# Performance work log

Measured on AMD Instinct MI355X. Metric: run time of the kernel, lower is better.

The kernel has to match this reference:

```python
import jax, jax.numpy as jnp
import numpy as np

N = 4608      # total nodes (48 graphs x 96 nodes)
B = 48
NPG = 96
D = 512       # vec_dim
XD = 16       # x_dim
E = N * 32    # GAT edges
L = 6         # GAT layers


def _w(k, shape, fan_in):
    return jax.random.normal(k, shape, jnp.float32) * (1.0 / np.sqrt(fan_in))


def setup_inputs() -> dict:
    key = jax.random.key(0)
    ks = jax.random.split(key, 24)
    x = jax.random.normal(ks[0], (N, XD), jnp.float32)
    xyz = jax.random.normal(ks[1], (N, 3), jnp.float32)
    edge_index = jax.random.randint(ks[2], (2, E), 0, N, dtype=jnp.int32)
    ptr = (jnp.arange(B + 1) * NPG).astype(jnp.int32)
    # complete graph with replacement per segment (torch.combinations order: i<=j)
    i, j = np.triu_indices(NPG)
    offs = (np.arange(B) * NPG)[:, None]
    cloud_edge_index = jnp.asarray(
        np.stack([(i[None, :] + offs).reshape(-1), (j[None, :] + offs).reshape(-1)]),
        jnp.int32)
    return {
        'x': x, 'edge_index': edge_index, 'ptr': ptr, 'xyz': xyz,
        'cloud_edge_index': cloud_edge_index,
        'x_proj_w': _w(ks[3], (XD, D), XD), 'x_proj_b': jnp.zeros((D,), jnp.float32),
        'gat_wl': _w(ks[4], (L, D, D), D), 'gat_bl': jnp.zeros((L, D), jnp.float32),
        'gat_wr': _w(ks[5], (L, D, D), D), 'gat_br': jnp.zeros((L, D), jnp.float32),
        'gat_att': _w(ks[6], (L, D), D), 'gat_bias': jnp.zeros((L, D), jnp.float32),
        'gat_ln_g': jnp.ones((L - 1, D), jnp.float32), 'gat_ln_b': jnp.zeros((L - 1, D), jnp.float32),
        'cg_xyz_w': _w(ks[7], (3, D), 3),
        'cg_bn_g': jnp.ones((D,), jnp.float32), 'cg_bn_b': jnp.zeros((D,), jnp.float32),
        'cg_lin1_w': _w(ks[8], (D, D), D), 'cg_lin1_b': jnp.zeros((D,), jnp.float32),
        'cg_ln_g': jnp.ones((D,), jnp.float32), 'cg_ln_b': jnp.zeros((D,), jnp.float32),
        'lin_w': _w(ks[9], (D, D), D), 'lin_b': jnp.zeros((D,), jnp.float32),
        'bn_g': jnp.ones((D,), jnp.float32), 'bn_b': jnp.zeros((D,), jnp.float32),
    }


def _batchnorm(t, g, b):
    mu = t.mean(0)
    v = ((t - mu) ** 2).mean(0)
    return (t - mu) / jnp.sqrt(v + 1e-5) * g + b


def _forward(x, edge_index, cloud_edge_index, x_proj_w, x_proj_b, gat_wl, gat_bl,
             gat_wr, gat_br, gat_att, gat_bias, gat_ln_g, gat_ln_b, cg_xyz_w,
             cg_bn_g, cg_bn_b, cg_lin1_w, cg_lin1_b, cg_ln_g, cg_ln_b,
             lin_w, lin_b, bn_g, bn_b, xyz):
    n = x.shape[0]
    h = x @ x_proj_w + x_proj_b  # [N, D]
    # ---- GATv2 stack (heads=1, self-loops added, eval mode: no dropout) ----
    loops = jnp.arange(n, dtype=edge_index.dtype)
    ei = jnp.concatenate([edge_index, jnp.stack([loops, loops])], axis=1)
    src, dst = ei[0], ei[1]
    xg = h
    for l in range(L):
        xl = xg @ gat_wl[l] + gat_bl[l]
        xr = xg @ gat_wr[l] + gat_br[l]
        e = jax.nn.leaky_relu(xl[src] + xr[dst], 0.2) @ gat_att[l]  # [E+N]
        m = jax.ops.segment_max(e, dst, num_segments=n)
        ew = jnp.exp(e - m[dst])
        den = jax.ops.segment_sum(ew, dst, num_segments=n)
        alpha = ew / den[dst]
        out = jax.ops.segment_sum(alpha[:, None] * xl[src], dst, num_segments=n) + gat_bias[l]
        if l < L - 1:
            # PyG LayerNorm, mode='graph', batch=None: normalize over all elements
            mu = out.mean()
            sd = jnp.sqrt(((out - mu) ** 2).mean())
            out = (out - mu) / (sd + 1e-5) * gat_ln_g[l] + gat_ln_b[l]
            out = jax.nn.relu(out)
        xg = out
    # ---- CloudGraph (complete graph gather-compute-scatter) ----
    a, b = cloud_edge_index[0], cloud_edge_index[1]
    rx = h[a] - h[b]          # [Ec, D]
    rz = xyz[a] - xyz[b]      # [Ec, 3]
    sq = (rz ** 2).sum(-1)
    dist = jnp.where(sq > 0, jnp.sqrt(jnp.where(sq > 0, sq, 1.0)), 0.0)
    w = jnp.exp(-dist)[:, None]
    p1 = jax.ops.segment_sum(jax.nn.relu((w * rx) @ cg_lin1_w + cg_lin1_b), a, num_segments=n)
    mu1 = p1.mean(-1, keepdims=True)
    v1 = ((p1 - mu1) ** 2).mean(-1, keepdims=True)
    ln1 = (p1 - mu1) / jnp.sqrt(v1 + 1e-5) * cg_ln_g + cg_ln_b
    p2 = jax.ops.segment_sum(jax.nn.relu(rz @ cg_xyz_w), a, num_segments=n)
    xc = h + ln1 + _batchnorm(p2, cg_bn_g, cg_bn_b)
    # ---- fuse + final norm ----
    return _batchnorm((h + xg + xc) @ lin_w + lin_b, bn_g, bn_b)


def reference(x, edge_index, ptr, xyz, cloud_edge_index, x_proj_w, x_proj_b,
              gat_wl, gat_bl, gat_wr, gat_br, gat_att, gat_bias, gat_ln_g,
              gat_ln_b, cg_xyz_w, cg_bn_g, cg_bn_b, cg_lin1_w, cg_lin1_b,
              cg_ln_g, cg_ln_b, lin_w, lin_b, bn_g, bn_b):
    return _forward(x, edge_index, cloud_edge_index, x_proj_w, x_proj_b, gat_wl,
                    gat_bl, gat_wr, gat_br, gat_att, gat_bias, gat_ln_g,
                    gat_ln_b, cg_xyz_w, cg_bn_g, cg_bn_b, cg_lin1_w, cg_lin1_b,
                    cg_ln_g, cg_ln_b, lin_w, lin_b, bn_g, bn_b, xyz)
```

## Files before the change

kernel.cpp:

```cpp
#include <hip/hip_runtime.h>
#include <hip/hip_bf16.h>

#define NN 4608
#define BG 48
#define NPG 96
#define DD 512
#define XDIM 16
#define EREAL 147456
#define NLAYER 6
#define NK 262144
#define TRIU 4656

typedef __hip_bfloat16 bf16;
typedef short short8 __attribute__((ext_vector_type(8)));
typedef short short4v __attribute__((ext_vector_type(4)));
typedef float f32x4 __attribute__((ext_vector_type(4)));

__device__ __forceinline__ float s2f(short s) {
  return __uint_as_float(((unsigned int)(unsigned short)s) << 16);
}
__device__ __forceinline__ short f2bs(float f) {
  bf16 h = __float2bfloat16(f);
  short s;
  __builtin_memcpy(&s, &h, 2);
  return s;
}

__global__ __launch_bounds__(256) void k_wt(const float* __restrict__ wl,
                                            const float* __restrict__ wr,
                                            const float* __restrict__ cg,
                                            const float* __restrict__ lin,
                                            bf16* __restrict__ Wt,
                                            int* __restrict__ counts,
                                            float* __restrict__ statsAll) {
  if (blockIdx.z == 0) {
    int id = (blockIdx.y * 16 + blockIdx.x) * 256 + threadIdx.x;
    if (id < NN) counts[id] = 0;
    if (id < 5 * 32) statsAll[id] = 0.f;
  }
  __shared__ float tile[32][33];
  int z = blockIdx.z;
  const float* src = (z < 6) ? wl + (size_t)z * NK
                   : (z < 12) ? wr + (size_t)(z - 6) * NK
                   : (z == 12) ? cg : lin;
  bf16* dst = Wt + (size_t)z * NK;
  int c = threadIdx.x & 31;
  int r0 = threadIdx.x >> 5;
  int bx = blockIdx.x * 32, by = blockIdx.y * 32;
#pragma unroll
  for (int i = 0; i < 4; i++) {
    int r = r0 + i * 8;
    tile[r][c] = src[(size_t)(by + r) * 512 + bx + c];
  }
  __syncthreads();
#pragma unroll
  for (int i = 0; i < 4; i++) {
    int r = r0 + i * 8;
    dst[(size_t)(bx + r) * 512 + by + c] = __float2bfloat16(tile[c][r]);
  }
}

__global__ void k_xproj(const float* __restrict__ x, const float* __restrict__ w,
                        const float* __restrict__ b, const int* __restrict__ ei,
                        const float* __restrict__ xyz,
                        bf16* __restrict__ h_bf, int* __restrict__ counts,
                        float* __restrict__ ep) {
  int i = blockIdx.x * blockDim.x + threadIdx.x;
  if (i >= NN * DD) return;
  if (i < EREAL) atomicAdd(&counts[ei[EREAL + i]], 1);
  if (i < NN * NPG) {
    int n = i / NPG, e = i - n * NPG;
    int p = n % NPG;
    if (e < NPG - p) {
      int g = n / NPG;
      int slot = g * TRIU + p * NPG - (p * (p - 1)) / 2 + e;
      int j = n + e;
      float dx = xyz[n * 3] - xyz[j * 3];
      float dy = xyz[n * 3 + 1] - xyz[j * 3 + 1];
      float dz = xyz[n * 3 + 2] - xyz[j * 3 + 2];
      float sq = dx * dx + dy * dy + dz * dz;
      float dist = (sq > 0.f) ? sqrtf(sq) : 0.f;
      float4 v;
      v.x = dx; v.y = dy; v.z = dz; v.w = __expf(-dist);
      *(float4*)&ep[(size_t)slot * 4] = v;
    }
  }
  int n = i >> 9, d = i & 511;
  float acc = b[d];
#pragma unroll
  for (int k = 0; k < XDIM; k++) acc += x[n * XDIM + k] * w[k * DD + d];
  h_bf[i] = __float2bfloat16(acc);
}

__global__ void k_scan(const int* __restrict__ counts, int* offsets, int* cursor) {
  __shared__ int part[256];
  __shared__ int pre[256];
  int t = threadIdx.x;
  int base = t * 18;
  int s = 0;
#pragma unroll
  for (int i = 0; i < 18; i++) s += counts[base + i];
  part[t] = s;
  __syncthreads();
  if (t == 0) {
    int r = 0;
    for (int i = 0; i < 256; i++) { pre[i] = r; r += part[i]; }
  }
  __syncthreads();
  int run = pre[t];
#pragma unroll
  for (int i = 0; i < 18; i++) {
    offsets[base + i] = run;
    cursor[base + i] = run;
    run += counts[base + i];
  }
  if (t == 0) offsets[NN] = EREAL;
}
__global__ void k_scatter(const int* __restrict__ ei, int* cursor, int* ssrc) {
  int e = blockIdx.x * blockDim.x + threadIdx.x;
  if (e < EREAL) {
    int s = ei[e], d = ei[EREAL + e];
    int pos = atomicAdd(&cursor[d], 1);
    ssrc[pos] = s;
  }
}

__global__ __launch_bounds__(256) void k_gemm(
    const bf16* __restrict__ Abf,
    const bf16* __restrict__ B0, const bf16* __restrict__ B1,
    const float* __restrict__ bias0, const float* __restrict__ bias1,
    float* __restrict__ C0, float* __restrict__ C1,
    bf16* __restrict__ Cb0, bf16* __restrict__ Cb1,
    const float* __restrict__ statsIn,
    const float* __restrict__ lng, const float* __restrict__ lnb,
    float* __restrict__ zptr, int zn,
    float* __restrict__ csum, float* __restrict__ csq) {
  if (zptr && blockIdx.x == 0 && blockIdx.y == 0 && blockIdx.z == 0) {
    for (int i = threadIdx.x; i < zn; i += 256) zptr[i] = 0.f;
  }
  __shared__ __align__(16) bf16 As[128 * 40];
  __shared__ __align__(16) bf16 Bs[64 * 40];
  __shared__ float cs[64], cq[64];
  const bf16* B = blockIdx.z ? B1 : B0;
  const float* bias = blockIdx.z ? bias1 : bias0;
  float* C = blockIdx.z ? C1 : C0;
  bf16* Cb = blockIdx.z ? Cb1 : Cb0;
  int tid = threadIdx.x;
  int m0 = blockIdx.x * 128, n0 = blockIdx.y * 64;
  int lane = tid & 63, wid = tid >> 6;
  int mh = (wid >> 1) * 64, nh = (wid & 1) * 32;
  int l15 = lane & 15, quad = lane >> 4;

  if (csum && tid < 64) { cs[tid] = 0.f; cq[tid] = 0.f; }

  float mu = 0.f, inv = 1.f;
  if (statsIn) {
    float s = 0.f, ss = 0.f;
#pragma unroll
    for (int i = 0; i < 16; i++) { s += statsIn[i]; ss += statsIn[16 + i]; }
    const float invM = 1.f / ((float)NN * (float)DD);
    mu = s * invM;
    float var = ss * invM - mu * mu;
    float sd = sqrtf(fmaxf(var, 0.f));
    inv = 1.f / (sd + 1e-5f);
  }

  f32x4 acc[4][2];
#pragma unroll
  for (int mt = 0; mt < 4; mt++)
#pragma unroll
    for (int nt = 0; nt < 2; nt++) acc[mt][nt] = (f32x4)0.f;

  for (int k0 = 0; k0 < 512; k0 += 32) {
    if (statsIn) {
#pragma unroll
      for (int it = 0; it < 2; it++) {
        int idx = tid + it * 256;
        int row = idx >> 2, kc = (idx & 3) * 8;
        short8 raw = *(const short8*)&Abf[(size_t)(m0 + row) * 512 + k0 + kc];
        float4 ga = *(const float4*)&lng[k0 + kc];
        float4 gb = *(const float4*)&lng[k0 + kc + 4];
        float4 ba = *(const float4*)&lnb[k0 + kc];
        float4 bb = *(const float4*)&lnb[k0 + kc + 4];
        float gg[8] = {ga.x, ga.y, ga.z, ga.w, gb.x, gb.y, gb.z, gb.w};
        float bv[8] = {ba.x, ba.y, ba.z, ba.w, bb.x, bb.y, bb.z, bb.w};
        short8 pk;
#pragma unroll
        for (int k = 0; k < 8; k++) {
          float t = fmaxf((s2f(raw[k]) - mu) * inv * gg[k] + bv[k], 0.f);
          pk[k] = f2bs(t);
        }
        *(short8*)&As[row * 40 + kc] = pk;
      }
    } else {
#pragma unroll
      for (int it = 0; it < 2; it++) {
        int idx = tid + it * 256;
        int row = idx >> 2, kc = (idx & 3) * 8;
        *(short8*)&As[row * 40 + kc] =
            *(const short8*)&Abf[(size_t)(m0 + row) * 512 + k0 + kc];
      }
    }
    {
      int row = tid >> 2, kc = (tid & 3) * 8;
      *(short8*)&Bs[row * 40 + kc] =
          *(const short8*)&B[(size_t)(n0 + row) * 512 + k0 + kc];
    }
    __syncthreads();
    short8 af[4], bfr[2];
#pragma unroll
    for (int mt = 0; mt < 4; mt++)
      af[mt] = *(const short8*)&As[(mh + mt * 16 + l15) * 40 + quad * 8];
#pragma unroll
    for (int nt = 0; nt < 2; nt++)
      bfr[nt] = *(const short8*)&Bs[(nh + nt * 16 + l15) * 40 + quad * 8];
#pragma unroll
    for (int mt = 0; mt < 4; mt++)
#pragma unroll
      for (int nt = 0; nt < 2; nt++)
        acc[mt][nt] = __builtin_amdgcn_mfma_f32_16x16x32_bf16(
            af[mt], bfr[nt], acc[mt][nt], 0, 0, 0);
    __syncthreads();
  }
  float colS[2] = {0.f, 0.f}, colQ[2] = {0.f, 0.f};
#pragma unroll
  for (int mt = 0; mt < 4; mt++) {
#pragma unroll
    for (int nt = 0; nt < 2; nt++) {
      int col = n0 + nh + nt * 16 + l15;
      float bv = bias ? bias[col] : 0.f;
#pragma unroll
      for (int r = 0; r < 4; r++) {
        int row = m0 + mh + mt * 16 + quad * 4 + r;
        float v = acc[mt][nt][r] + bv;
        if (C) C[(size_t)row * 512 + col] = v;
        if (Cb) Cb[(size_t)row * 512 + col] = __float2bfloat16(v);
        if (csum) { colS[nt] += v; colQ[nt] += v * v; }
      }
    }
  }
  if (csum) {
#pragma unroll
    for (int nt = 0; nt < 2; nt++) {
      atomicAdd(&cs[nh + nt * 16 + l15], colS[nt]);
      atomicAdd(&cq[nh + nt * 16 + l15], colQ[nt]);
    }
    __syncthreads();
    if (tid < 64) {
      atomicAdd(&csum[n0 + tid], cs[tid]);
      atomicAdd(&csq[n0 + tid], cq[tid]);
    }
  }
}

__global__ __launch_bounds__(256) void k_gat_edge(const bf16* __restrict__ xl,
                                                  const bf16* __restrict__ xr,
                                                  const float* __restrict__ att,
                                                  const float* __restrict__ bias,
                                                  const int* __restrict__ offs,
                                                  const int* __restrict__ ssrc,
                                                  bf16* __restrict__ out,
                                                  float* __restrict__ statsOut) {
  __shared__ float redS[4], redSS[4];
  int wave = (blockIdx.x * blockDim.x + threadIdx.x) >> 6;
  int lane = threadIdx.x & 63;
  int wid = threadIdx.x >> 6;
  if (wave < NN) {
    int n = wave;
    int base = lane * 8;
    float xrv[8], attv[8], acc[8];
    short8 xr8 = *(const short8*)&xr[(size_t)n * 512 + base];
#pragma unroll
    for (int k = 0; k < 8; k++) {
      xrv[k] = s2f(xr8[k]);
      attv[k] = att[base + k];
    }
    float m0, lsum;
    {
      short8 a8 = *(const short8*)&xl[(size_t)n * 512 + base];
      float sc0 = 0.f;
#pragma unroll
      for (int k = 0; k < 8; k++) {
        float v = s2f(a8[k]);
        acc[k] = v;
        float t = v + xrv[k];
        t = (t > 0.f) ? t : 0.2f * t;
        sc0 += attv[k] * t;
      }
#pragma unroll
      for (int off = 32; off >= 1; off >>= 1) sc0 += __shfl_xor(sc0, off, 64);
      m0 = sc0;
      lsum = 1.f;
    }
    int e0 = offs[n], e1 = offs[n + 1];
    int e = e0;
    for (; e + 3 < e1; e += 4) {
      int s0 = ssrc[e], s1 = ssrc[e + 1], s2 = ssrc[e + 2], s3 = ssrc[e + 3];
      short8 a0 = *(const short8*)&xl[(size_t)s0 * 512 + base];
      short8 a1 = *(const short8*)&xl[(size_t)s1 * 512 + base];
      short8 a2 = *(const short8*)&xl[(size_t)s2 * 512 + base];
      short8 a3 = *(const short8*)&xl[(size_t)s3 * 512 + base];
      float x0[8], x1[8], x2[8], x3[8];
      float c0 = 0.f, c1 = 0.f, c2 = 0.f, c3 = 0.f;
#pragma unroll
      for (int k = 0; k < 8; k++) {
        float v0 = s2f(a0[k]), v1 = s2f(a1[k]), v2 = s2f(a2[k]), v3 = s2f(a3[k]);
        x0[k] = v0; x1[k] = v1; x2[k] = v2; x3[k] = v3;
        float t0 = v0 + xrv[k]; t0 = (t0 > 0.f) ? t0 : 0.2f * t0; c0 += attv[k] * t0;
        float t1 = v1 + xrv[k]; t1 = (t1 > 0.f) ? t1 : 0.2f * t1; c1 += attv[k] * t1;
        float t2 = v2 + xrv[k]; t2 = (t2 > 0.f) ? t2 : 0.2f * t2; c2 += attv[k] * t2;
        float t3 = v3 + xrv[k]; t3 = (t3 > 0.f) ? t3 : 0.2f * t3; c3 += attv[k] * t3;
      }
#pragma unroll
      for (int off = 32; off >= 1; off >>= 1) {
        c0 += __shfl_xor(c0, off, 64);
        c1 += __shfl_xor(c1, off, 64);
        c2 += __shfl_xor(c2, off, 64);
        c3 += __shfl_xor(c3, off, 64);
      }
      float p0 = __expf(c0 - m0), p1 = __expf(c1 - m0);
      float p2 = __expf(c2 - m0), p3 = __expf(c3 - m0);
      lsum += p0 + p1 + p2 + p3;
#pragma unroll
      for (int k = 0; k < 8; k++)
        acc[k] += p0 * x0[k] + p1 * x1[k] + p2 * x2[k] + p3 * x3[k];
    }
    for (; e < e1; ++e) {
      int s0 = ssrc[e];
      short8 a8 = *(const short8*)&xl[(size_t)s0 * 512 + base];
      float x0[8];
      float sc0 = 0.f;
#pragma unroll
      for (int k = 0; k < 8; k++) {
        float v0 = s2f(a8[k]);
        x0[k] = v0;
        float t0 = v0 + xrv[k];
        t0 = (t0 > 0.f) ? t0 : 0.2f * t0;
        sc0 += attv[k] * t0;
      }
#pragma unroll
      for (int off = 32; off >= 1; off >>= 1) sc0 += __shfl_xor(sc0, off, 64);
      float p0 = __expf(sc0 - m0);
      lsum += p0;
#pragma unroll
      for (int k = 0; k < 8; k++) acc[k] += p0 * x0[k];
    }
    float inv = 1.f / lsum;
    float o[8];
    float s = 0.f, ss = 0.f;
    short8 o8;
#pragma unroll
    for (int k = 0; k < 8; k++) {
      o[k] = acc[k] * inv + bias[base + k];
      s += o[k];
      ss += o[k] * o[k];
      o8[k] = f2bs(o[k]);
    }
    *(short8*)&out[(size_t)n * 512 + base] = o8;
    if (statsOut) {
#pragma unroll
      for (int off = 32; off >= 1; off >>= 1) {
        s += __shfl_xor(s, off, 64);
        ss += __shfl_xor(ss, off, 64);
      }
      if (lane == 0) { redS[wid] = s; redSS[wid] = ss; }
    }
  }
  if (statsOut) {
    __syncthreads();
    if (threadIdx.x == 0) {
      float a = redS[0] + redS[1] + redS[2] + redS[3];
      float b = redSS[0] + redSS[1] + redSS[2] + redSS[3];
      int slot = blockIdx.x & 15;
      atomicAdd(&statsOut[slot], a);
      atomicAdd(&statsOut[16 + slot], b);
    }
  }
}

__global__ __launch_bounds__(256) void k_cloud(const bf16* __restrict__ g1,
                                               const float* __restrict__ ep,
                                               const float* __restrict__ lin1b,
                                               const float* __restrict__ w3,
                                               float* __restrict__ p1,
                                               float* __restrict__ p2) {
  int w = (blockIdx.x * blockDim.x + threadIdx.x) >> 6;
  int lane = threadIdx.x & 63;
  if (w >= NN) return;
  int hf = w & 1;
  int pi = w >> 1;
  int g = pi / 48, pp = pi % 48;
  int d0 = hf * 256 + lane * 4;
  float4 bb = *(const float4*)&lin1b[d0];
  float4 w30 = *(const float4*)&w3[d0];
  float4 w31 = *(const float4*)&w3[512 + d0];
  float4 w32 = *(const float4*)&w3[1024 + d0];
  float bbv[4] = {bb.x, bb.y, bb.z, bb.w};
  float w0v[4] = {w30.x, w30.y, w30.z, w30.w};
  float w1v[4] = {w31.x, w31.y, w31.z, w31.w};
  float w2v[4] = {w32.x, w32.y, w32.z, w32.w};

#pragma unroll
  for (int half = 0; half < 2; half++) {
    int p = half ? (NPG - 1 - pp) : pp;
    int n = g * NPG + p;
    int cnt = NPG - p;
    int slot0 = g * TRIU + p * NPG - (p * (p - 1)) / 2;
    float gi[4], a1[4], a2[4];
    short4v gi4 = *(const short4v*)&g1[(size_t)n * 512 + d0];
#pragma unroll
    for (int k = 0; k < 4; k++) {
      gi[k] = s2f(gi4[k]);
      a1[k] = 0.f;
      a2[k] = 0.f;
    }
    int e = 0;
    for (; e + 1 < cnt; e += 2) {
      float4 pa = *(const float4*)&ep[(size_t)(slot0 + e) * 4];
      float4 pb = *(const float4*)&ep[(size_t)(slot0 + e + 1) * 4];
      short4v ga = *(const short4v*)&g1[(size_t)(n + e) * 512 + d0];
      short4v gb = *(const short4v*)&g1[(size_t)(n + e + 1) * 512 + d0];
#pragma unroll
      for (int k = 0; k < 4; k++) {
        float t = fmaf(pa.w, gi[k] - s2f(ga[k]), bbv[k]);
        a1[k] += fmaxf(t, 0.f);
        float u = fmaf(pb.w, gi[k] - s2f(gb[k]), bbv[k]);
        a1[k] += fmaxf(u, 0.f);
        float t2 = pa.x * w0v[k] + pa.y * w1v[k] + pa.z * w2v[k];
        a2[k] += fmaxf(t2, 0.f);
        float u2 = pb.x * w0v[k] + pb.y * w1v[k] + pb.z * w2v[k];
        a2[k] += fmaxf(u2, 0.f);
      }
    }
    if (e < cnt) {
      float4 pa = *(const float4*)&ep[(size_t)(slot0 + e) * 4];
      short4v ga = *(const short4v*)&g1[(size_t)(n + e) * 512 + d0];
#pragma unroll
      for (int k = 0; k < 4; k++) {
        float t = fmaf(pa.w, gi[k] - s2f(ga[k]), bbv[k]);
        a1[k] += fmaxf(t, 0.f);
        float t2 = pa.x * w0v[k] + pa.y * w1v[k] + pa.z * w2v[k];
        a2[k] += fmaxf(t2, 0.f);
      }
    }
    float4 o1, o2;
    o1.x = a1[0]; o1.y = a1[1]; o1.z = a1[2]; o1.w = a1[3];
    o2.x = a2[0]; o2.y = a2[1]; o2.z = a2[2]; o2.w = a2[3];
    *(float4*)&p1[(size_t)n * 512 + d0] = o1;
    *(float4*)&p2[(size_t)n * 512 + d0] = o2;
  }
}

__global__ __launch_bounds__(256) void k_cloud_epi(
    const float* __restrict__ p1, const float* __restrict__ p2,
    const bf16* __restrict__ h_bf, const bf16* __restrict__ xg_bf,
    const float* __restrict__ colsum, const float* __restrict__ colsq,
    const float* __restrict__ lng, const float* __restrict__ lnb,
    const float* __restrict__ bng, const float* __restrict__ bnb,
    bf16* __restrict__ s_bf, float* __restrict__ zptr) {
  if (blockIdx.x == 0) {
    for (int i = threadIdx.x; i < 1024; i += 256) zptr[i] = 0.f;
  }
  int wave = (blockIdx.x * blockDim.x + threadIdx.x) >> 6;
  int lane = threadIdx.x & 63;
  if (wave >= NN) return;
  int n = wave;
  size_t rb = (size_t)n * 512 + lane * 8;
  int base = lane * 8;
  float v[8];
  float s = 0.f;
#pragma unroll
  for (int k = 0; k < 8; k++) {
    v[k] = p1[rb + k];
    s += v[k];
  }
#pragma unroll
  for (int off = 32; off >= 1; off >>= 1) s += __shfl_xor(s, off, 64);
  float mu = s * (1.f / 512.f);
  float ss = 0.f;
#pragma unroll
  for (int k = 0; k < 8; k++) {
    float t = v[k] - mu;
    ss += t * t;
  }
#pragma unroll
  for (int off = 32; off >= 1; off >>= 1) ss += __shfl_xor(ss, off, 64);
  float inv = 1.f / sqrtf(ss * (1.f / 512.f) + 1e-5f);
  short8 hb = *(const short8*)&h_bf[rb];
  short8 xb = *(const short8*)&xg_bf[rb];
  short8 o8;
#pragma unroll
  for (int k = 0; k < 8; k++) {
    int d = base + k;
    float ln1 = (v[k] - mu) * inv * lng[d] + lnb[d];
    float cmu = colsum[d] * (1.f / NN);
    float cvar = colsq[d] * (1.f / NN) - cmu * cmu;
    float cinv = 1.f / sqrtf(fmaxf(cvar, 0.f) + 1e-5f);
    float bnv = (p2[rb + k] - cmu) * cinv * bng[d] + bnb[d];
    float out = 2.f * s2f(hb[k]) + s2f(xb[k]) + ln1 + bnv;
    o8[k] = f2bs(out);
  }
  *(short8*)&s_bf[rb] = o8;
}

__global__ void k_col_reduce(const float* __restrict__ x, float* colsum, float* colsq) {
  int r0 = blockIdx.x * 128;
  int c0 = threadIdx.x;
  float s0 = 0.f, q0 = 0.f, s1 = 0.f, q1 = 0.f;
  for (int r = r0; r < r0 + 128; ++r) {
    float v = x[(size_t)r * 512 + c0];
    s0 += v;
    q0 += v * v;
    float w = x[(size_t)r * 512 + c0 + 256];
    s1 += w;
    q1 += w * w;
  }
  atomicAdd(&colsum[c0], s0);
  atomicAdd(&colsq[c0], q0);
  atomicAdd(&colsum[c0 + 256], s1);
  atomicAdd(&colsq[c0 + 256], q1);
}
__global__ void k_bn_out(const float* __restrict__ y, const float* __restrict__ colsum,
                         const float* __restrict__ colsq, const float* __restrict__ g,
                         const float* __restrict__ b, float* __restrict__ out) {
  int i = blockIdx.x * blockDim.x + threadIdx.x;
  if (i >= NN * DD) return;
  int d = i & 511;
  float mu = colsum[d] * (1.f / NN);
  float var = colsq[d] * (1.f / NN) - mu * mu;
  float inv = 1.f / sqrtf(fmaxf(var, 0.f) + 1e-5f);
  out[i] = (y[i] - mu) * inv * g[d] + b[d];
}

extern "C" void kernel_launch(void* const* d_in, const int* in_sizes, int n_in,
                              void* d_out, int out_size, void* d_ws, size_t ws_size,
                              hipStream_t stream) {
  const float* x = (const float*)d_in[0];
  const int* ei = (const int*)d_in[1];
  const float* xyz = (const float*)d_in[3];
  const float* x_proj_w = (const float*)d_in[5];
  const float* x_proj_b = (const float*)d_in[6];
  const float* gat_wl = (const float*)d_in[7];
  const float* gat_bl = (const float*)d_in[8];
  const float* gat_wr = (const float*)d_in[9];
  const float* gat_br = (const float*)d_in[10];
  const float* gat_att = (const float*)d_in[11];
  const float* gat_bias = (const float*)d_in[12];
  const float* gat_ln_g = (const float*)d_in[13];
  const float* gat_ln_b = (const float*)d_in[14];
  const float* cg_xyz_w = (const float*)d_in[15];
  const float* cg_bn_g = (const float*)d_in[16];
  const float* cg_bn_b = (const float*)d_in[17];
  const float* cg_lin1_w = (const float*)d_in[18];
  const float* cg_lin1_b = (const float*)d_in[19];
  const float* cg_ln_g = (const float*)d_in[20];
  const float* cg_ln_b = (const float*)d_in[21];
  const float* lin_w = (const float*)d_in[22];
  const float* lin_b = (const float*)d_in[23];
  const float* bn_g = (const float*)d_in[24];
  const float* bn_b = (const float*)d_in[25];

  const size_t ND = (size_t)NN * DD;
  char* w = (char*)d_ws;
  float* p1 = (float*)w;       w += ND * 4;
  float* p2 = (float*)w;       w += ND * 4;
  bf16* h_bf = (bf16*)w;       w += ND * 2;
  bf16* xg_bf = (bf16*)w;      w += ND * 2;
  bf16* xl_bf = (bf16*)w;      w += ND * 2;
  bf16* xr_bf = (bf16*)w;      w += ND * 2;
  bf16* Wt = (bf16*)w;         w += (size_t)14 * NK * 2;
  float* eparam = (float*)w;   w += (size_t)BG * TRIU * 16;
  int* counts = (int*)w;       w += NN * 4;
  int* offs = (int*)w;         w += (NN + 4) * 4;
  int* cursor = (int*)w;       w += NN * 4;
  int* ssrc = (int*)w;         w += EREAL * 4;
  float* statsAll = (float*)w; w += 5 * 32 * 4;
  float* colsum = (float*)w;   w += 512 * 4;
  float* colsq = (float*)w;    w += 512 * 4;
  float* colsum2 = (float*)w;  w += 512 * 4;
  float* colsq2 = (float*)w;   w += 512 * 4;
  float* y = p1;
  bf16* g1_bf = xl_bf;
  bf16* s_bf = h_bf;

  const int TPB = 256;
  const int ND_BLK = (int)((ND + TPB - 1) / TPB);

  k_wt<<<dim3(16, 16, 14), TPB, 0, stream>>>(gat_wl, gat_wr, cg_lin1_w, lin_w, Wt,
                                             counts, statsAll);
  k_xproj<<<ND_BLK, TPB, 0, stream>>>(x, x_proj_w, x_proj_b, ei, xyz, h_bf,
                                      counts, eparam);
  k_scan<<<1, 256, 0, stream>>>(counts, offs, cursor);
  k_scatter<<<(EREAL + TPB - 1) / TPB, TPB, 0, stream>>>(ei, cursor, ssrc);

  for (int l = 0; l < NLAYER; l++) {
    const bf16* A = (l == 0) ? h_bf : xg_bf;
    const float* sIn = (l > 0) ? statsAll + 32 * (l - 1) : nullptr;
    const float* lg = (l > 0) ? gat_ln_g + (l - 1) * DD : nullptr;
    const float* lb = (l > 0) ? gat_ln_b + (l - 1) * DD : nullptr;
    k_gemm<<<dim3(36, 8, 2), TPB, 0, stream>>>(
        A, Wt + (size_t)l * NK, Wt + (size_t)(6 + l) * NK,
        gat_bl + l * DD, gat_br + l * DD, nullptr, nullptr, xl_bf, xr_bf,
        sIn, lg, lb, nullptr, 0, nullptr, nullptr);
    float* sOut = (l < NLAYER - 1) ? statsAll + 32 * l : nullptr;
    k_gat_edge<<<NN / 4, TPB, 0, stream>>>(xl_bf, xr_bf, gat_att + l * DD,
                                           gat_bias + l * DD, offs, ssrc,
                                           xg_bf, sOut);
  }

  k_gemm<<<dim3(36, 8, 1), TPB, 0, stream>>>(
      h_bf, Wt + (size_t)12 * NK, Wt + (size_t)12 * NK, nullptr, nullptr,
      nullptr, nullptr, g1_bf, g1_bf, nullptr, nullptr, nullptr,
      colsum, 1024, nullptr, nullptr);
  k_cloud<<<NN / 4, TPB, 0, stream>>>(g1_bf, eparam, cg_lin1_b, cg_xyz_w, p1, p2);
  k_col_reduce<<<36, 256, 0, stream>>>(p2, colsum, colsq);
  k_cloud_epi<<<NN / 4, TPB, 0, stream>>>(p1, p2, h_bf, xg_bf, colsum, colsq,
                                          cg_ln_g, cg_ln_b, cg_bn_g, cg_bn_b,
                                          s_bf, colsum2);

  k_gemm<<<dim3(36, 8, 1), TPB, 0, stream>>>(
      s_bf, Wt + (size_t)13 * NK, Wt + (size_t)13 * NK, lin_b, lin_b,
      y, y, nullptr, nullptr, nullptr, nullptr, nullptr,
      nullptr, 0, colsum2, colsq2);
  k_bn_out<<<ND_BLK, TPB, 0, stream>>>(y, colsum2, colsq2, bn_g, bn_b,
                                       (float*)d_out);
}
```

Before: 598.7 us.

## Store GAT source features in fp8 and split cloud kernel across more waves

Result: no change. 597.8 us (-0.2%).

```diff
diff --git a/kernel.cpp b/kernel.cpp
--- a/kernel.cpp
+++ b/kernel.cpp
@@ -13,8 +13,8 @@
 
 typedef __hip_bfloat16 bf16;
 typedef short short8 __attribute__((ext_vector_type(8)));
-typedef short short4v __attribute__((ext_vector_type(4)));
 typedef float f32x4 __attribute__((ext_vector_type(4)));
+typedef float f32x2 __attribute__((ext_vector_type(2)));
 
 __device__ __forceinline__ float s2f(short s) {
   return __uint_as_float(((unsigned int)(unsigned short)s) << 16);
@@ -24,6 +24,14 @@
   short s;
   __builtin_memcpy(&s, &h, 2);
   return s;
+}
+__device__ __forceinline__ unsigned char f2f8(float v) {
+  return (unsigned char)(__builtin_amdgcn_cvt_pk_fp8_f32(v, v, 0, false) & 0xff);
+}
+__device__ __forceinline__ void f8x4(unsigned int w, float* o) {
+  f32x2 a = __builtin_amdgcn_cvt_pk_f32_fp8(w, false);
+  f32x2 b = __builtin_amdgcn_cvt_pk_f32_fp8(w, true);
+  o[0] = a[0]; o[1] = a[1]; o[2] = b[0]; o[3] = b[1];
 }
 
 __global__ __launch_bounds__(256) void k_wt(const float* __restrict__ wl,
@@ -131,6 +139,7 @@
     const float* __restrict__ bias0, const float* __restrict__ bias1,
     float* __restrict__ C0, float* __restrict__ C1,
     bf16* __restrict__ Cb0, bf16* __restrict__ Cb1,
+    unsigned char* __restrict__ Cf8_0, unsigned char* __restrict__ Cf8_1,
     const float* __restrict__ statsIn,
     const float* __restrict__ lng, const float* __restrict__ lnb,
     float* __restrict__ zptr, int zn,
@@ -145,6 +154,7 @@
   const float* bias = blockIdx.z ? bias1 : bias0;
   float* C = blockIdx.z ? C1 : C0;
   bf16* Cb = blockIdx.z ? Cb1 : Cb0;
+  unsigned char* Cf8 = blockIdx.z ? Cf8_1 : Cf8_0;
   int tid = threadIdx.x;
   int m0 = blockIdx.x * 128, n0 = blockIdx.y * 64;
   int lane = tid & 63, wid = tid >> 6;
@@ -235,6 +245,7 @@
         float v = acc[mt][nt][r] + bv;
         if (C) C[(size_t)row * 512 + col] = v;
         if (Cb) Cb[(size_t)row * 512 + col] = __float2bfloat16(v);
+        if (Cf8) Cf8[(size_t)row * 512 + col] = f2f8(v);
         if (csum) { colS[nt] += v; colQ[nt] += v * v; }
       }
     }
@@ -253,7 +264,7 @@
   }
 }
 
-__global__ __launch_bounds__(256) void k_gat_edge(const bf16* __restrict__ xl,
+__global__ __launch_bounds__(256) void k_gat_edge(const unsigned char* __restrict__ xl8,
                                                   const bf16* __restrict__ xr,
                                                   const float* __restrict__ att,
                                                   const float* __restrict__ bias,
@@ -277,13 +288,15 @@
     }
     float m0, lsum;
     {
-      short8 a8 = *(const short8*)&xl[(size_t)n * 512 + base];
+      uint2 q = *(const uint2*)&xl8[(size_t)n * 512 + base];
+      float xs[8];
+      f8x4(q.x, xs);
+      f8x4(q.y, xs + 4);
       float sc0 = 0.f;
 #pragma unroll
       for (int k = 0; k < 8; k++) {
-        float v = s2f(a8[k]);
-        acc[k] = v;
-        float t = v + xrv[k];
+        acc[k] = xs[k];
+        float t = xs[k] + xrv[k];
         t = (t > 0.f) ? t : 0.2f * t;
         sc0 += attv[k] * t;
       }
@@ -296,20 +309,22 @@
     int e = e0;
     for (; e + 3 < e1; e += 4) {
       int s0 = ssrc[e], s1 = ssrc[e + 1], s2 = ssrc[e + 2], s3 = ssrc[e + 3];
-      short8 a0 = *(const short8*)&xl[(size_t)s0 * 512 + base];
-      short8 a1 = *(const short8*)&xl[(size_t)s1 * 512 + base];
-      short8 a2 = *(const short8*)&xl[(size_t)s2 * 512 + base];
-      short8 a3 = *(const short8*)&xl[(size_t)s3 * 512 + base];
+      uint2 q0 = *(const uint2*)&xl8[(size_t)s0 * 512 + base];
+      uint2 q1 = *(const uint2*)&xl8[(size_t)s1 * 512 + base];
+      uint2 q2 = *(const uint2*)&xl8[(size_t)s2 * 512 + base];
+      uint2 q3 = *(const uint2*)&xl8[(size_t)s3 * 512 + base];
       float x0[8], x1[8], x2[8], x3[8];
+      f8x4(q0.x, x0); f8x4(q0.y, x0 + 4);
+      f8x4(q1.x, x1); f8x4(q1.y, x1 + 4);
+      f8x4(q2.x, x2); f8x4(q2.y, x2 + 4);
+      f8x4(q3.x, x3); f8x4(q3.y, x3 + 4);
       float c0 = 0.f, c1 = 0.f, c2 = 0.f, c3 = 0.f;
 #pragma unroll
       for (int k = 0; k < 8; k++) {
-        float v0 = s2f(a0[k]), v1 = s2f(a1[k]), v2 = s2f(a2[k]), v3 = s2f(a3[k]);
-        x0[k] = v0; x1[k] = v1; x2[k] = v2; x3[k] = v3;
-        float t0 = v0 + xrv[k]; t0 = (t0 > 0.f) ? t0 : 0.2f * t0; c0 += attv[k] * t0;
-        float t1 = v1 + xrv[k]; t1 = (t1 > 0.f) ? t1 : 0.2f * t1; c1 += attv[k] * t1;
-        float t2 = v2 + xrv[k]; t2 = (t2 > 0.f) ? t2 : 0.2f * t2; c2 += attv[k] * t2;
-        float t3 = v3 + xrv[k]; t3 = (t3 > 0.f) ? t3 : 0.2f * t3; c3 += attv[k] * t3;
+        float t0 = x0[k] + xrv[k]; t0 = (t0 > 0.f) ? t0 : 0.2f * t0; c0 += attv[k] * t0;
+        float t1 = x1[k] + xrv[k]; t1 = (t1 > 0.f) ? t1 : 0.2f * t1; c1 += attv[k] * t1;
+        float t2 = x2[k] + xrv[k]; t2 = (t2 > 0.f) ? t2 : 0.2f * t2; c2 += attv[k] * t2;
+        float t3 = x3[k] + xrv[k]; t3 = (t3 > 0.f) ? t3 : 0.2f * t3; c3 += attv[k] * t3;
       }
 #pragma unroll
       for (int off = 32; off >= 1; off >>= 1) {
@@ -327,14 +342,14 @@
     }
     for (; e < e1; ++e) {
       int s0 = ssrc[e];
-      short8 a8 = *(const short8*)&xl[(size_t)s0 * 512 + base];
+      uint2 q = *(const uint2*)&xl8[(size_t)s0 * 512 + base];
       float x0[8];
+      f8x4(q.x, x0);
+      f8x4(q.y, x0 + 4);
       float sc0 = 0.f;
 #pragma unroll
       for (int k = 0; k < 8; k++) {
-        float v0 = s2f(a8[k]);
-        x0[k] = v0;
-        float t0 = v0 + xrv[k];
+        float t0 = x0[k] + xrv[k];
         t0 = (t0 > 0.f) ? t0 : 0.2f * t0;
         sc0 += attv[k] * t0;
       }
@@ -386,19 +401,15 @@
                                                float* __restrict__ p2) {
   int w = (blockIdx.x * blockDim.x + threadIdx.x) >> 6;
   int lane = threadIdx.x & 63;
-  if (w >= NN) return;
-  int hf = w & 1;
-  int pi = w >> 1;
+  if (w >= NN * 2) return;
+  int qf = w & 3;
+  int pi = w >> 2;
   int g = pi / 48, pp = pi % 48;
-  int d0 = hf * 256 + lane * 4;
-  float4 bb = *(const float4*)&lin1b[d0];
-  float4 w30 = *(const float4*)&w3[d0];
-  float4 w31 = *(const float4*)&w3[512 + d0];
-  float4 w32 = *(const float4*)&w3[1024 + d0];
-  float bbv[4] = {bb.x, bb.y, bb.z, bb.w};
-  float w0v[4] = {w30.x, w30.y, w30.z, w30.w};
-  float w1v[4] = {w31.x, w31.y, w31.z, w31.w};
-  float w2v[4] = {w32.x, w32.y, w32.z, w32.w};
+  int d0 = qf * 128 + lane * 2;
+  float bb0 = lin1b[d0], bb1 = lin1b[d0 + 1];
+  float w00 = w3[d0], w01 = w3[d0 + 1];
+  float w10 = w3[512 + d0], w11 = w3[512 + d0 + 1];
+  float w20 = w3[1024 + d0], w21 = w3[1024 + d0 + 1];
 
 #pragma unroll
   for (int half = 0; half < 2; half++) {
@@ -406,48 +417,40 @@
     int n = g * NPG + p;
     int cnt = NPG - p;
     int slot0 = g * TRIU + p * NPG - (p * (p - 1)) / 2;
-    float gi[4], a1[4], a2[4];
-    short4v gi4 = *(const short4v*)&g1[(size_t)n * 512 + d0];
-#pragma unroll
-    for (int k = 0; k < 4; k++) {
-      gi[k] = s2f(gi4[k]);
-      a1[k] = 0.f;
-      a2[k] = 0.f;
-    }
+    unsigned int giw = *(const unsigned int*)&g1[(size_t)n * 512 + d0];
+    float gi0 = s2f((short)(giw & 0xffff));
+    float gi1 = s2f((short)(giw >> 16));
+    float a10 = 0.f, a11 = 0.f, a20 = 0.f, a21 = 0.f;
     int e = 0;
     for (; e + 1 < cnt; e += 2) {
       float4 pa = *(const float4*)&ep[(size_t)(slot0 + e) * 4];
       float4 pb = *(const float4*)&ep[(size_t)(slot0 + e + 1) * 4];
-      short4v ga = *(const short4v*)&g1[(size_t)(n + e) * 512 + d0];
-      short4v gb = *(const short4v*)&g1[(size_t)(n + e + 1) * 512 + d0];
-#pragma unroll
-      for (int k = 0; k < 4; k++) {
-        float t = fmaf(pa.w, gi[k] - s2f(ga[k]), bbv[k]);
-        a1[k] += fmaxf(t, 0.f);
-        float u = fmaf(pb.w, gi[k] - s2f(gb[k]), bbv[k]);
-        a1[k] += fmaxf(u, 0.f);
-        float t2 = pa.x * w0v[k] + pa.y * w1v[k] + pa.z * w2v[k];
-        a2[k] += fmaxf(t2, 0.f);
-        float u2 = pb.x * w0v[k] + pb.y * w1v[k] + pb.z * w2v[k];
-        a2[k] += fmaxf(u2, 0.f);
-      }
+      unsigned int gaw = *(const unsigned int*)&g1[(size_t)(n + e) * 512 + d0];
+      unsigned int gbw = *(const unsigned int*)&g1[(size_t)(n + e + 1) * 512 + d0];
+      float t;
+      t = fmaf(pa.w, gi0 - s2f((short)(gaw & 0xffff)), bb0); a10 += fmaxf(t, 0.f);
+      t = fmaf(pa.w, gi1 - s2f((short)(gaw >> 16)), bb1);    a11 += fmaxf(t, 0.f);
+      t = fmaf(pb.w, gi0 - s2f((short)(gbw & 0xffff)), bb0); a10 += fmaxf(t, 0.f);
+      t = fmaf(pb.w, gi1 - s2f((short)(gbw >> 16)), bb1);    a11 += fmaxf(t, 0.f);
+      t = pa.x * w00 + pa.y * w10 + pa.z * w20; a20 += fmaxf(t, 0.f);
+      t = pa.x * w01 + pa.y * w11 + pa.z * w21; a21 += fmaxf(t, 0.f);
+      t = pb.x * w00 + pb.y * w10 + pb.z * w20; a20 += fmaxf(t, 0.f);
+      t = pb.x * w01 + pb.y * w11 + pb.z * w21; a21 += fmaxf(t, 0.f);
     }
     if (e < cnt) {
       float4 pa = *(const float4*)&ep[(size_t)(slot0 + e) * 4];
-      short4v ga = *(const short4v*)&g1[(size_t)(n + e) * 512 + d0];
-#pragma unroll
-      for (int k = 0; k < 4; k++) {
-        float t = fmaf(pa.w, gi[k] - s2f(ga[k]), bbv[k]);
-        a1[k] += fmaxf(t, 0.f);
-        float t2 = pa.x * w0v[k] + pa.y * w1v[k] + pa.z * w2v[k];
-        a2[k] += fmaxf(t2, 0.f);
-      }
-    }
-    float4 o1, o2;
-    o1.x = a1[0]; o1.y = a1[1]; o1.z = a1[2]; o1.w = a1[3];
-    o2.x = a2[0]; o2.y = a2[1]; o2.z = a2[2]; o2.w = a2[3];
-    *(float4*)&p1[(size_t)n * 512 + d0] = o1;
-    *(float4*)&p2[(size_t)n * 512 + d0] = o2;
+      unsigned int gaw = *(const unsigned int*)&g1[(size_t)(n + e) * 512 + d0];
+      float t;
+      t = fmaf(pa.w, gi0 - s2f((short)(gaw & 0xffff)), bb0); a10 += fmaxf(t, 0.f);
+      t = fmaf(pa.w, gi1 - s2f((short)(gaw >> 16)), bb1);    a11 += fmaxf(t, 0.f);
+      t = pa.x * w00 + pa.y * w10 + pa.z * w20; a20 += fmaxf(t, 0.f);
+      t = pa.x * w01 + pa.y * w11 + pa.z * w21; a21 += fmaxf(t, 0.f);
+    }
+    float2 o1, o2;
+    o1.x = a10; o1.y = a11;
+    o2.x = a20; o2.y = a21;
+    *(float2*)&p1[(size_t)n * 512 + d0] = o1;
+    *(float2*)&p2[(size_t)n * 512 + d0] = o2;
   }
 }
 
@@ -566,8 +569,9 @@
   float* p2 = (float*)w;       w += ND * 4;
   bf16* h_bf = (bf16*)w;       w += ND * 2;
   bf16* xg_bf = (bf16*)w;      w += ND * 2;
-  bf16* xl_bf = (bf16*)w;      w += ND * 2;
+  bf16* g1_bf = (bf16*)w;      w += ND * 2;
   bf16* xr_bf = (bf16*)w;      w += ND * 2;
+  unsigned char* xl_f8 = (unsigned char*)w; w += ND;
   bf16* Wt = (bf16*)w;         w += (size_t)14 * NK * 2;
   float* eparam = (float*)w;   w += (size_t)BG * TRIU * 16;
   int* counts = (int*)w;       w += NN * 4;
@@ -580,7 +584,6 @@
   float* colsum2 = (float*)w;  w += 512 * 4;
   float* colsq2 = (float*)w;   w += 512 * 4;
   float* y = p1;
-  bf16* g1_bf = xl_bf;
   bf16* s_bf = h_bf;
 
   const int TPB = 256;
@@ -600,19 +603,19 @@
     const float* lb = (l > 0) ? gat_ln_b + (l - 1) * DD : nullptr;
     k_gemm<<<dim3(36, 8, 2), TPB, 0, stream>>>(
         A, Wt + (size_t)l * NK, Wt + (size_t)(6 + l) * NK,
-        gat_bl + l * DD, gat_br + l * DD, nullptr, nullptr, xl_bf, xr_bf,
-        sIn, lg, lb, nullptr, 0, nullptr, nullptr);
+        gat_bl + l * DD, gat_br + l * DD, nullptr, nullptr, nullptr, xr_bf,
+        xl_f8, nullptr, sIn, lg, lb, nullptr, 0, nullptr, nullptr);
     float* sOut = (l < NLAYER - 1) ? statsAll + 32 * l : nullptr;
-    k_gat_edge<<<NN / 4, TPB, 0, stream>>>(xl_bf, xr_bf, gat_att + l * DD,
+    k_gat_edge<<<NN / 4, TPB, 0, stream>>>(xl_f8, xr_bf, gat_att + l * DD,
                                            gat_bias + l * DD, offs, ssrc,
                                            xg_bf, sOut);
   }
 
   k_gemm<<<dim3(36, 8, 1), TPB, 0, stream>>>(
       h_bf, Wt + (size_t)12 * NK, Wt + (size_t)12 * NK, nullptr, nullptr,
-      nullptr, nullptr, g1_bf, g1_bf, nullptr, nullptr, nullptr,
+      nullptr, nullptr, g1_bf, g1_bf, nullptr, nullptr, nullptr, nullptr, nullptr,
       colsum, 1024, nullptr, nullptr);
-  k_cloud<<<NN / 4, TPB, 0, stream>>>(g1_bf, eparam, cg_lin1_b, cg_xyz_w, p1, p2);
+  k_cloud<<<NN / 2, TPB, 0, stream>>>(g1_bf, eparam, cg_lin1_b, cg_xyz_w, p1, p2);
   k_col_reduce<<<36, 256, 0, stream>>>(p2, colsum, colsq);
   k_cloud_epi<<<NN / 4, TPB, 0, stream>>>(p1, p2, h_bf, xg_bf, colsum, colsq,
                                           cg_ln_g, cg_ln_b, cg_bn_g, cg_bn_b,
@@ -620,7 +623,7 @@
 
   k_gemm<<<dim3(36, 8, 1), TPB, 0, stream>>>(
       s_bf, Wt + (size_t)13 * NK, Wt + (size_t)13 * NK, lin_b, lin_b,
-      y, y, nullptr, nullptr, nullptr, nullptr, nullptr,
+      y, y, nullptr, nullptr, nullptr, nullptr, nullptr, nullptr, nullptr,
       nullptr, 0, colsum2, colsq2);
   k_bn_out<<<ND_BLK, TPB, 0, stream>>>(y, colsum2, colsq2, bn_g, bn_b,
                                        (float*)d_out);
```

## Store GAT source features in FP8, prefetch neighbor batches, fuse column stats into cloud kernel

Applied to the files above, without the earlier changes.

After: 679.8 us. +13.5%, slower.

```diff
diff --git a/kernel.cpp b/kernel.cpp
--- a/kernel.cpp
+++ b/kernel.cpp
@@ -15,6 +15,7 @@
 typedef short short8 __attribute__((ext_vector_type(8)));
 typedef short short4v __attribute__((ext_vector_type(4)));
 typedef float f32x4 __attribute__((ext_vector_type(4)));
+typedef float f32x2 __attribute__((ext_vector_type(2)));
 
 __device__ __forceinline__ float s2f(short s) {
   return __uint_as_float(((unsigned int)(unsigned short)s) << 16);
@@ -24,6 +25,14 @@
   short s;
   __builtin_memcpy(&s, &h, 2);
   return s;
+}
+__device__ __forceinline__ unsigned char f2f8(float v) {
+  return (unsigned char)(__builtin_amdgcn_cvt_pk_fp8_f32(v, v, 0, false) & 0xff);
+}
+__device__ __forceinline__ void f8x4(unsigned int w, float* o) {
+  f32x2 a = __builtin_amdgcn_cvt_pk_f32_fp8(w, false);
+  f32x2 b = __builtin_amdgcn_cvt_pk_f32_fp8(w, true);
+  o[0] = a[0]; o[1] = a[1]; o[2] = b[0]; o[3] = b[1];
 }
 
 __global__ __launch_bounds__(256) void k_wt(const float* __restrict__ wl,
@@ -131,6 +140,7 @@
     const float* __restrict__ bias0, const float* __restrict__ bias1,
     float* __restrict__ C0, float* __restrict__ C1,
     bf16* __restrict__ Cb0, bf16* __restrict__ Cb1,
+    unsigned char* __restrict__ Cf8_0, unsigned char* __restrict__ Cf8_1,
     const float* __restrict__ statsIn,
     const float* __restrict__ lng, const float* __restrict__ lnb,
     float* __restrict__ zptr, int zn,
@@ -145,6 +155,7 @@
   const float* bias = blockIdx.z ? bias1 : bias0;
   float* C = blockIdx.z ? C1 : C0;
   bf16* Cb = blockIdx.z ? Cb1 : Cb0;
+  unsigned char* Cf8 = blockIdx.z ? Cf8_1 : Cf8_0;
   int tid = threadIdx.x;
   int m0 = blockIdx.x * 128, n0 = blockIdx.y * 64;
   int lane = tid & 63, wid = tid >> 6;
@@ -235,6 +246,7 @@
         float v = acc[mt][nt][r] + bv;
         if (C) C[(size_t)row * 512 + col] = v;
         if (Cb) Cb[(size_t)row * 512 + col] = __float2bfloat16(v);
+        if (Cf8) Cf8[(size_t)row * 512 + col] = f2f8(v);
         if (csum) { colS[nt] += v; colQ[nt] += v * v; }
       }
     }
@@ -253,7 +265,7 @@
   }
 }
 
-__global__ __launch_bounds__(256) void k_gat_edge(const bf16* __restrict__ xl,
+__global__ __launch_bounds__(256) void k_gat_edge(const unsigned char* __restrict__ xl8,
                                                   const bf16* __restrict__ xr,
                                                   const float* __restrict__ att,
                                                   const float* __restrict__ bias,
@@ -277,13 +289,15 @@
     }
     float m0, lsum;
     {
-      short8 a8 = *(const short8*)&xl[(size_t)n * 512 + base];
+      uint2 q = *(const uint2*)&xl8[(size_t)n * 512 + base];
+      float xs[8];
+      f8x4(q.x, xs);
+      f8x4(q.y, xs + 4);
       float sc0 = 0.f;
 #pragma unroll
       for (int k = 0; k < 8; k++) {
-        float v = s2f(a8[k]);
-        acc[k] = v;
-        float t = v + xrv[k];
+        acc[k] = xs[k];
+        float t = xs[k] + xrv[k];
         t = (t > 0.f) ? t : 0.2f * t;
         sc0 += attv[k] * t;
       }
@@ -293,23 +307,41 @@
       lsum = 1.f;
     }
     int e0 = offs[n], e1 = offs[n + 1];
-    int e = e0;
-    for (; e + 3 < e1; e += 4) {
-      int s0 = ssrc[e], s1 = ssrc[e + 1], s2 = ssrc[e + 2], s3 = ssrc[e + 3];
-      short8 a0 = *(const short8*)&xl[(size_t)s0 * 512 + base];
-      short8 a1 = *(const short8*)&xl[(size_t)s1 * 512 + base];
-      short8 a2 = *(const short8*)&xl[(size_t)s2 * 512 + base];
-      short8 a3 = *(const short8*)&xl[(size_t)s3 * 512 + base];
+    int cnt = e1 - e0;
+    int nbat = (cnt + 3) >> 2;
+    uint2 q[4];
+#pragma unroll
+    for (int j = 0; j < 4; j++) {
+      int idx = (j < cnt) ? ssrc[e0 + j] : n;
+      q[j] = *(const uint2*)&xl8[(size_t)idx * 512 + base];
+    }
+    for (int b = 0; b < nbat; b++) {
+      int rem = cnt - b * 4;
+      uint2 qn[4];
+      if (b + 1 < nbat) {
+        int eb = e0 + (b + 1) * 4;
+        int remn = cnt - (b + 1) * 4;
+#pragma unroll
+        for (int j = 0; j < 4; j++) {
+          int idx = (j < remn) ? ssrc[eb + j] : n;
+          qn[j] = *(const uint2*)&xl8[(size_t)idx * 512 + base];
+        }
+      } else {
+#pragma unroll
+        for (int j = 0; j < 4; j++) qn[j] = q[j];
+      }
       float x0[8], x1[8], x2[8], x3[8];
+      f8x4(q[0].x, x0); f8x4(q[0].y, x0 + 4);
+      f8x4(q[1].x, x1); f8x4(q[1].y, x1 + 4);
+      f8x4(q[2].x, x2); f8x4(q[2].y, x2 + 4);
+      f8x4(q[3].x, x3); f8x4(q[3].y, x3 + 4);
       float c0 = 0.f, c1 = 0.f, c2 = 0.f, c3 = 0.f;
 #pragma unroll
       for (int k = 0; k < 8; k++) {
-        float v0 = s2f(a0[k]), v1 = s2f(a1[k]), v2 = s2f(a2[k]), v3 = s2f(a3[k]);
-        x0[k] = v0; x1[k] = v1; x2[k] = v2; x3[k] = v3;
-        float t0 = v0 + xrv[k]; t0 = (t0 > 0.f) ? t0 : 0.2f * t0; c0 += attv[k] * t0;
-        float t1 = v1 + xrv[k]; t1 = (t1 > 0.f) ? t1 : 0.2f * t1; c1 += attv[k] * t1;
-        float t2 = v2 + xrv[k]; t2 = (t2 > 0.f) ? t2 : 0.2f * t2; c2 += attv[k] * t2;
-        float t3 = v3 + xrv[k]; t3 = (t3 > 0.f) ? t3 : 0.2f * t3; c3 += attv[k] * t3;
+        float t0 = x0[k] + xrv[k]; t0 = (t0 > 0.f) ? t0 : 0.2f * t0; c0 += attv[k] * t0;
+        float t1 = x1[k] + xrv[k]; t1 = (t1 > 0.f) ? t1 : 0.2f * t1; c1 += attv[k] * t1;
+        float t2 = x2[k] + xrv[k]; t2 = (t2 > 0.f) ? t2 : 0.2f * t2; c2 += attv[k] * t2;
+        float t3 = x3[k] + xrv[k]; t3 = (t3 > 0.f) ? t3 : 0.2f * t3; c3 += attv[k] * t3;
       }
 #pragma unroll
       for (int off = 32; off >= 1; off >>= 1) {
@@ -318,32 +350,16 @@
         c2 += __shfl_xor(c2, off, 64);
         c3 += __shfl_xor(c3, off, 64);
       }
-      float p0 = __expf(c0 - m0), p1 = __expf(c1 - m0);
-      float p2 = __expf(c2 - m0), p3 = __expf(c3 - m0);
+      float p0 = (rem > 0) ? __expf(c0 - m0) : 0.f;
+      float p1 = (rem > 1) ? __expf(c1 - m0) : 0.f;
+      float p2 = (rem > 2) ? __expf(c2 - m0) : 0.f;
+      float p3 = (rem > 3) ? __expf(c3 - m0) : 0.f;
       lsum += p0 + p1 + p2 + p3;
 #pragma unroll
       for (int k = 0; k < 8; k++)
         acc[k] += p0 * x0[k] + p1 * x1[k] + p2 * x2[k] + p3 * x3[k];
-    }
-    for (; e < e1; ++e) {
-      int s0 = ssrc[e];
-      short8 a8 = *(const short8*)&xl[(size_t)s0 * 512 + base];
-      float x0[8];
-      float sc0 = 0.f;
-#pragma unroll
-      for (int k = 0; k < 8; k++) {
-        float v0 = s2f(a8[k]);
-        x0[k] = v0;
-        float t0 = v0 + xrv[k];
-        t0 = (t0 > 0.f) ? t0 : 0.2f * t0;
-        sc0 += attv[k] * t0;
-      }
-#pragma unroll
-      for (int off = 32; off >= 1; off >>= 1) sc0 += __shfl_xor(sc0, off, 64);
-      float p0 = __expf(sc0 - m0);
-      lsum += p0;
-#pragma unroll
-      for (int k = 0; k < 8; k++) acc[k] += p0 * x0[k];
+#pragma unroll
+      for (int j = 0; j < 4; j++) q[j] = qn[j];
     }
     float inv = 1.f / lsum;
     float o[8];
@@ -383,10 +399,14 @@
                                                const float* __restrict__ lin1b,
                                                const float* __restrict__ w3,
                                                float* __restrict__ p1,
-                                               float* __restrict__ p2) {
+                                               float* __restrict__ p2,
+                                               float* __restrict__ colsum,
+                                               float* __restrict__ colsq) {
+  __shared__ float cS[512], cQ[512];
+  for (int i = threadIdx.x; i < 512; i += 256) { cS[i] = 0.f; cQ[i] = 0.f; }
+  __syncthreads();
   int w = (blockIdx.x * blockDim.x + threadIdx.x) >> 6;
   int lane = threadIdx.x & 63;
-  if (w >= NN) return;
   int hf = w & 1;
   int pi = w >> 1;
   int g = pi / 48, pp = pi % 48;
@@ -448,6 +468,16 @@
     o2.x = a2[0]; o2.y = a2[1]; o2.z = a2[2]; o2.w = a2[3];
     *(float4*)&p1[(size_t)n * 512 + d0] = o1;
     *(float4*)&p2[(size_t)n * 512 + d0] = o2;
+#pragma unroll
+    for (int k = 0; k < 4; k++) {
+      atomicAdd(&cS[d0 + k], a2[k]);
+      atomicAdd(&cQ[d0 + k], a2[k] * a2[k]);
+    }
+  }
+  __syncthreads();
+  for (int i = threadIdx.x; i < 512; i += 256) {
+    atomicAdd(&colsum[i], cS[i]);
+    atomicAdd(&colsq[i], cQ[i]);
   }
 }
 
@@ -503,23 +533,6 @@
   *(short8*)&s_bf[rb] = o8;
 }
 
-__global__ void k_col_reduce(const float* __restrict__ x, float* colsum, float* colsq) {
-  int r0 = blockIdx.x * 128;
-  int c0 = threadIdx.x;
-  float s0 = 0.f, q0 = 0.f, s1 = 0.f, q1 = 0.f;
-  for (int r = r0; r < r0 + 128; ++r) {
-    float v = x[(size_t)r * 512 + c0];
-    s0 += v;
-    q0 += v * v;
-    float w = x[(size_t)r * 512 + c0 + 256];
-    s1 += w;
-    q1 += w * w;
-  }
-  atomicAdd(&colsum[c0], s0);
-  atomicAdd(&colsq[c0], q0);
-  atomicAdd(&colsum[c0 + 256], s1);
-  atomicAdd(&colsq[c0 + 256], q1);
-}
 __global__ void k_bn_out(const float* __restrict__ y, const float* __restrict__ colsum,
                          const float* __restrict__ colsq, const float* __restrict__ g,
                          const float* __restrict__ b, float* __restrict__ out) {
@@ -566,8 +579,9 @@
   float* p2 = (float*)w;       w += ND * 4;
   bf16* h_bf = (bf16*)w;       w += ND * 2;
   bf16* xg_bf = (bf16*)w;      w += ND * 2;
-  bf16* xl_bf = (bf16*)w;      w += ND * 2;
+  bf16* g1_bf = (bf16*)w;      w += ND * 2;
   bf16* xr_bf = (bf16*)w;      w += ND * 2;
+  unsigned char* xl_f8 = (unsigned char*)w; w += ND;
   bf16* Wt = (bf16*)w;         w += (size_t)14 * NK * 2;
   float* eparam = (float*)w;   w += (size_t)BG * TRIU * 16;
   int* counts = (int*)w;       w += NN * 4;
@@ -580,7 +594,6 @@
   float* colsum2 = (float*)w;  w += 512 * 4;
   float* colsq2 = (float*)w;   w += 512 * 4;
   float* y = p1;
-  bf16* g1_bf = xl_bf;
   bf16* s_bf = h_bf;
 
   const int TPB = 256;
@@ -600,27 +613,27 @@
     const float* lb = (l > 0) ? gat_ln_b + (l - 1) * DD : nullptr;
     k_gemm<<<dim3(36, 8, 2), TPB, 0, stream>>>(
         A, Wt + (size_t)l * NK, Wt + (size_t)(6 + l) * NK,
-        gat_bl + l * DD, gat_br + l * DD, nullptr, nullptr, xl_bf, xr_bf,
-        sIn, lg, lb, nullptr, 0, nullptr, nullptr);
+        gat_bl + l * DD, gat_br + l * DD, nullptr, nullptr, nullptr, xr_bf,
+        xl_f8, nullptr, sIn, lg, lb, nullptr, 0, nullptr, nullptr);
     float* sOut = (l < NLAYER - 1) ? statsAll + 32 * l : nullptr;
-    k_gat_edge<<<NN / 4, TPB, 0, stream>>>(xl_bf, xr_bf, gat_att + l * DD,
+    k_gat_edge<<<NN / 4, TPB, 0, stream>>>(xl_f8, xr_bf, gat_att + l * DD,
                                            gat_bias + l * DD, offs, ssrc,
                                            xg_bf, sOut);
   }
 
   k_gemm<<<dim3(36, 8, 1), TPB, 0, stream>>>(
       h_bf, Wt + (size_t)12 * NK, Wt + (size_t)12 * NK, nullptr, nullptr,
-      nullptr, nullptr, g1_bf, g1_bf, nullptr, nullptr, nullptr,
+      nullptr, nullptr, g1_bf, g1_bf, nullptr, nullptr, nullptr, nullptr, nullptr,
       colsum, 1024, nullptr, nullptr);
-  k_cloud<<<NN / 4, TPB, 0, stream>>>(g1_bf, eparam, cg_lin1_b, cg_xyz_w, p1, p2);
-  k_col_reduce<<<36, 256, 0, stream>>>(p2, colsum, colsq);
+  k_cloud<<<NN / 4, TPB, 0, stream>>>(g1_bf, eparam, cg_lin1_b, cg_xyz_w, p1, p2,
+                                      colsum, colsq);
   k_cloud_epi<<<NN / 4, TPB, 0, stream>>>(p1, p2, h_bf, xg_bf, colsum, colsq,
                                           cg_ln_g, cg_ln_b, cg_bn_g, cg_bn_b,
                                           s_bf, colsum2);
 
   k_gemm<<<dim3(36, 8, 1), TPB, 0, stream>>>(
       s_bf, Wt + (size_t)13 * NK, Wt + (size_t)13 * NK, lin_b, lin_b,
-      y, y, nullptr, nullptr, nullptr, nullptr, nullptr,
+      y, y, nullptr, nullptr, nullptr, nullptr, nullptr, nullptr, nullptr,
       nullptr, 0, colsum2, colsq2);
   k_bn_out<<<ND_BLK, TPB, 0, stream>>>(y, colsum2, colsq2, bn_g, bn_b,
                                        (float*)d_out);
```
